# Performance work log

Hardware: AMD Instinct MI355X
Metric: run time of the kernel (lower is better)

The kernel has to match this reference:

```python
import jax, jax.numpy as jnp
import numpy as np

B, L, IN_DIMS = 256, 512, 64
UNITS, OUT_STEPS, OUT_DIMS = 256, 64, 32
KSIZE = 5


def setup_inputs() -> dict:
    key = jax.random.key(0)
    ks = jax.random.split(key, 14)
    s = lambda k, shp: jax.random.normal(k, shp, dtype=jnp.float32) * 0.05
    return {
        "inputs": jax.random.normal(ks[0], (B, L, IN_DIMS), dtype=jnp.float32),
        "conv_k": s(ks[1], (KSIZE, IN_DIMS, UNITS)),   # WIO layout
        "conv_b": s(ks[2], (UNITS,)),
        "enc_W": s(ks[3], (UNITS, 4 * UNITS)),          # kernel (input after CNN has UNITS channels)
        "enc_U": s(ks[4], (UNITS, 4 * UNITS)),          # recurrent kernel
        "enc_b": s(ks[5], (4 * UNITS,)),
        "cell_W": s(ks[6], (UNITS, 4 * UNITS)),
        "cell_U": s(ks[7], (UNITS, 4 * UNITS)),
        "cell_b": s(ks[8], (4 * UNITS,)),
        "fore_W": s(ks[9], (UNITS, OUT_DIMS)),
        "fore_b": s(ks[10], (OUT_DIMS,)),
        "back_W": s(ks[11], (UNITS, IN_DIMS)),
        "back_b": s(ks[12], (IN_DIMS,)),
    }


def _lstm_step(W, U, b, h, c, x_t):
    # Keras gate order: i, f, g(candidate), o
    z = x_t @ W + h @ U + b
    i, f, g, o = jnp.split(z, 4, axis=-1)
    c_new = jax.nn.sigmoid(f) * c + jax.nn.sigmoid(i) * jnp.tanh(g)
    h_new = jax.nn.sigmoid(o) * jnp.tanh(c_new)
    return h_new, c_new


def _forward(inputs, conv_k, conv_b, enc_W, enc_U, enc_b,
             cell_W, cell_U, cell_b, fore_W, fore_b, back_W, back_b):
    # Conv1D 'same', relu
    x = jax.lax.conv_general_dilated(
        inputs, conv_k, window_strides=(1,), padding="SAME",
        dimension_numbers=("NWC", "WIO", "NWC"))
    x = jax.nn.relu(x + conv_b)

    # Encoder LSTM (dropout inactive at inference)
    h0 = jnp.zeros((x.shape[0], UNITS), x.dtype)
    c0 = jnp.zeros((x.shape[0], UNITS), x.dtype)

    def enc_step(carry, x_t):
        h, c = carry
        h, c = _lstm_step(enc_W, enc_U, enc_b, h, c, x_t)
        return (h, c), h
    (h_T, c_T), seq = jax.lax.scan(enc_step, (h0, c0), jnp.swapaxes(x, 0, 1))
    backcast_seq = jnp.swapaxes(seq, 0, 1)  # [B, L, UNITS]

    def dec_step(carry, _):
        h, c = carry
        h, c = _lstm_step(cell_W, cell_U, cell_b, h, c, h)
        return (h, c), h
    _, outs = jax.lax.scan(dec_step, (h_T, c_T), None, length=OUT_STEPS)
    forecast_seq = jnp.swapaxes(outs, 0, 1)  # [B, OUT_STEPS, UNITS]

    forecast = forecast_seq @ fore_W + fore_b   # [B, OUT_STEPS, OUT_DIMS]
    backcast = backcast_seq @ back_W + back_b   # [B, L, IN_DIMS]
    return forecast, backcast


def reference(inputs, conv_k, conv_b, enc_W, enc_U, enc_b,
              cell_W, cell_U, cell_b, fore_W, fore_b, back_W, back_b):
    return _forward(inputs, conv_k, conv_b, enc_W, enc_U, enc_b,
                    cell_W, cell_U, cell_b, fore_W, fore_b, back_W, back_b)
```

## Files before the change

### kernel.cpp

```cpp
#include <hip/hip_runtime.h>
#include <stdint.h>

typedef unsigned short u16;
typedef __attribute__((ext_vector_type(8))) short bf16x8;
typedef __attribute__((ext_vector_type(4))) float fx4;
typedef __attribute__((ext_vector_type(2))) unsigned int u32x2;

#define MFMA16(a, b, c) __builtin_amdgcn_mfma_f32_16x16x32_bf16((a), (b), (c), 0, 0, 0)

#define OFF_X      0u
#define OFF_H      67108864u
#define RING_OFF   134348800u
#define OFF_ENCWT  142737408u
#define OFF_ENCUT  143261696u
#define OFF_CELLT  143785984u
#define OFF_CONVKT 144310272u
#define OFF_BWT    144474112u
#define OFF_FWT    144506880u
#define OFF_BAR    144523264u

#define POLL_BUDGET (1 << 25)

__device__ __forceinline__ u16 f2bf(float f) {
    uint32_t u = __builtin_bit_cast(uint32_t, f);
    u += 0x7FFFu + ((u >> 16) & 1u);
    return (u16)(u >> 16);
}
__device__ __forceinline__ float sigm(float x) { return 1.0f / (1.0f + __expf(-x)); }
__device__ __forceinline__ float tanh_f(float x) { return 1.0f - 2.0f / (__expf(2.0f * x) + 1.0f); }
__device__ __forceinline__ void vmcnt0() { asm volatile("s_waitcnt vmcnt(0)" ::: "memory"); }

__global__ void zero_kernel(unsigned char* ws) {
    int i = blockIdx.x * blockDim.x + threadIdx.x;
    uint32_t* h0 = (uint32_t*)(ws + OFF_H);
    for (int k = i; k < 32768; k += 16384) h0[k] = 0u;
    if (i < 256) ((uint32_t*)(ws + OFF_BAR))[i] = 0u;
}

__global__ void prep_kernel(const float* enc_W, const float* enc_U, const float* cell_W,
                            const float* cell_U, const float* conv_k, const float* back_W,
                            const float* fore_W, unsigned char* ws) {
    u16* encWt = (u16*)(ws + OFF_ENCWT);
    u16* encUt = (u16*)(ws + OFF_ENCUT);
    u16* cellT = (u16*)(ws + OFF_CELLT);
    u16* convKt = (u16*)(ws + OFF_CONVKT);
    u16* bwt = (u16*)(ws + OFF_BWT);
    u16* fwt = (u16*)(ws + OFF_FWT);
    int idx = blockIdx.x * blockDim.x + threadIdx.x;
    int stride = gridDim.x * blockDim.x;
    for (int i = idx; i < 262144; i += stride) {
        int n = i >> 8, k = i & 255;
        encWt[i] = f2bf(enc_W[k * 1024 + n]);
        encUt[i] = f2bf(enc_U[k * 1024 + n]);
        cellT[i] = f2bf(cell_W[k * 1024 + n] + cell_U[k * 1024 + n]);
    }
    for (int i = idx; i < 81920; i += stride) {
        int u = i / 320, rem = i - u * 320;
        convKt[i] = f2bf(conv_k[rem * 256 + u]);
    }
    for (int i = idx; i < 16384; i += stride) {
        int n = i >> 8, k = i & 255;
        bwt[i] = f2bf(back_W[k * 64 + n]);
    }
    for (int i = idx; i < 8192; i += stride) {
        int n = i >> 8, k = i & 255;
        fwt[i] = f2bf(fore_W[k * 32 + n]);
    }
}

__global__ __launch_bounds__(256) void conv_kernel(const float* __restrict__ in,
                                                   const float* __restrict__ conv_b,
                                                   unsigned char* ws) {
    const u16* kt = (const u16*)(ws + OFF_CONVKT);
    u16* xout = (u16*)(ws + OFF_X);
    int w = threadIdx.x >> 6, lane = threadIdx.x & 63;
    int m = lane & 15, q = lane >> 4;
    int mt = blockIdx.x * 4 + w;
    int r0 = mt * 16;
    int b = r0 >> 9;
    int l0 = r0 & 511;

    fx4 acc[16];
#pragma unroll
    for (int nt = 0; nt < 16; ++nt) acc[nt] = (fx4){0.f, 0.f, 0.f, 0.f};

#pragma unroll
    for (int s = 0; s < 10; ++s) {
        int k0 = s * 32 + q * 8;
        int kk = k0 >> 6, c = k0 & 63;
        int l2 = l0 + m + kk - 2;
        bf16x8 af = {0, 0, 0, 0, 0, 0, 0, 0};
        if (l2 >= 0 && l2 < 512) {
            const float* src = in + (((b << 9) + l2) << 6) + c;
            fx4 f0 = *(const fx4*)src;
            fx4 f1 = *(const fx4*)(src + 4);
            af[0] = (short)f2bf(f0[0]); af[1] = (short)f2bf(f0[1]);
            af[2] = (short)f2bf(f0[2]); af[3] = (short)f2bf(f0[3]);
            af[4] = (short)f2bf(f1[0]); af[5] = (short)f2bf(f1[1]);
            af[6] = (short)f2bf(f1[2]); af[7] = (short)f2bf(f1[3]);
        }
#pragma unroll
        for (int nt = 0; nt < 16; ++nt) {
            bf16x8 bf = *(const bf16x8*)(kt + (nt * 16 + m) * 320 + k0);
            acc[nt] = MFMA16(af, bf, acc[nt]);
        }
    }
#pragma unroll
    for (int nt = 0; nt < 16; ++nt) {
        int u = nt * 16 + m;
        float bias = conv_b[u];
#pragma unroll
        for (int r = 0; r < 4; ++r) {
            float v = acc[nt][r] + bias;
            v = v > 0.f ? v : 0.f;
            int row = r0 + q * 4 + r;
            xout[row * 256 + u] = f2bf(v);
        }
    }
}

__global__ __launch_bounds__(256, 1) void enc_fused(const float* __restrict__ enc_b,
                                                    unsigned char* ws) {
    __shared__ u16 hbuf[1024];
    int tid = threadIdx.x;
    int w = tid >> 6, lane = tid & 63, m = lane & 15, q = lane >> 4;
    int bid = blockIdx.x;
    u16* H = (u16*)(ws + OFF_H);
    int budget = POLL_BUDGET;

    if (bid >= 64) {
        int idx = bid - 64, g = idx & 15, p = idx >> 4;
        int b0 = g * 16;
        int un0 = p * 64 + w * 16;
        const u16* encWt = (const u16*)(ws + OFF_ENCWT);
        const u16* xbf = (const u16*)(ws + OFF_X);
        float* ringg = (float*)(ws + RING_OFF + (size_t)g * 524288u);
        int* hbar = (int*)(ws + OFF_BAR + g * 64);
        int* pz = (int*)(ws + OFF_BAR + g * 64 + 32);

        bf16x8 wfr[4][8];
        float bi[4];
#pragma unroll
        for (int j = 0; j < 4; ++j) {
            int row = j * 256 + un0 + m;
            bi[j] = enc_b[row];
#pragma unroll
            for (int ks = 0; ks < 8; ++ks)
                wfr[j][ks] = *(const bf16x8*)(encWt + row * 256 + ks * 32 + q * 8);
        }
        const u16* xrow = xbf + (size_t)(b0 + m) * (512 * 256) + q * 8;
        bf16x8 xa[8];
#pragma unroll
        for (int s = 0; s < 8; ++s) xa[s] = *(const bf16x8*)(xrow + s * 32);

        for (int t = 0; t < 512; ++t) {
            fx4 a0 = (fx4){bi[0], bi[0], bi[0], bi[0]};
            fx4 a1 = (fx4){bi[1], bi[1], bi[1], bi[1]};
            fx4 a2 = (fx4){bi[2], bi[2], bi[2], bi[2]};
            fx4 a3 = (fx4){bi[3], bi[3], bi[3], bi[3]};
#pragma unroll
            for (int ks = 0; ks < 8; ++ks) {
                a0 = MFMA16(xa[ks], wfr[0][ks], a0);
                a1 = MFMA16(xa[ks], wfr[1][ks], a1);
                a2 = MFMA16(xa[ks], wfr[2][ks], a2);
                a3 = MFMA16(xa[ks], wfr[3][ks], a3);
            }
            float* zs = ringg + (t & 7) * 16384 + (un0 + m) * 16 + q * 4;
            asm volatile("global_store_dwordx4 %0, %1, off sc0 sc1" :: "v"(zs), "v"(a0) : "memory");
            asm volatile("global_store_dwordx4 %0, %1, off sc0 sc1" :: "v"(zs + 4096), "v"(a1) : "memory");
            asm volatile("global_store_dwordx4 %0, %1, off sc0 sc1" :: "v"(zs + 8192), "v"(a2) : "memory");
            asm volatile("global_store_dwordx4 %0, %1, off sc0 sc1" :: "v"(zs + 12288), "v"(a3) : "memory");
            if (t < 511) {
                const u16* xA = xrow + (size_t)(t + 1) * 256;
#pragma unroll
                for (int s = 0; s < 8; ++s) xa[s] = *(const bf16x8*)(xA + s * 32);
                if (tid == 0 && t >= 7) {
                    int tgt = 4 * (t - 6);
                    while (__hip_atomic_load(hbar, __ATOMIC_RELAXED, __HIP_MEMORY_SCOPE_AGENT) < tgt
                           && --budget > 0) {}
                }
            }
            vmcnt0();
            __syncthreads();
            if (tid == 0)
                __hip_atomic_fetch_add(pz, 1, __ATOMIC_RELAXED, __HIP_MEMORY_SCOPE_AGENT);
        }
        return;
    }

    int g = bid & 15, p = bid >> 4;
    int b0 = g * 16;
    int un0 = p * 64 + w * 16;
    const u16* encUt = (const u16*)(ws + OFF_ENCUT);
    const float* ringg = (const float*)(ws + RING_OFF + (size_t)g * 524288u);
    float* csaveg = (float*)(ws + OFF_X + (size_t)g * 4194304u);
    int* hbar = (int*)(ws + OFF_BAR + g * 64);
    int* pz = (int*)(ws + OFF_BAR + g * 64 + 32);

    bf16x8 ufrag[4][8];
#pragma unroll
    for (int gi = 0; gi < 4; ++gi) {
#pragma unroll
        for (int s = 0; s < 8; ++s)
            ufrag[gi][s] = *(const bf16x8*)(encUt + (gi * 256 + un0 + m) * 256 + s * 32 + q * 8);
    }
    float creg[4] = {0.f, 0.f, 0.f, 0.f};

    for (int t = 0; t < 512; ++t) {
        if (lane == 0) {
            int tgtz = 4 * (t + 1), tgth = 4 * t;
            while (--budget > 0) {
                int vz = __hip_atomic_load(pz, __ATOMIC_RELAXED, __HIP_MEMORY_SCOPE_AGENT);
                int vh = __hip_atomic_load(hbar, __ATOMIC_RELAXED, __HIP_MEMORY_SCOPE_AGENT);
                if (vz >= tgtz && vh >= tgth) break;
            }
        }
        asm volatile("" ::: "memory");

        const u16* hA = H + (size_t)t * 65536 + (b0 + m) * 256 + q * 8;
        bf16x8 ha[8];
#pragma unroll
        for (int s = 0; s < 8; ++s) ha[s] = *(const bf16x8*)(hA + s * 32);
        const float* zb = ringg + (t & 7) * 16384 + (un0 + m) * 16 + q * 4;
        fx4 z0, z1, z2, z3;
        asm volatile("global_load_dwordx4 %0, %1, off sc0 sc1" : "=v"(z0) : "v"(zb));
        asm volatile("global_load_dwordx4 %0, %1, off sc0 sc1" : "=v"(z1) : "v"(zb + 4096));
        asm volatile("global_load_dwordx4 %0, %1, off sc0 sc1" : "=v"(z2) : "v"(zb + 8192));
        asm volatile("global_load_dwordx4 %0, %1, off sc0 sc1" : "=v"(z3) : "v"(zb + 12288));

        fx4 acc[4];
#pragma unroll
        for (int gi = 0; gi < 4; ++gi) acc[gi] = (fx4){0.f, 0.f, 0.f, 0.f};
#pragma unroll
        for (int s = 0; s < 8; ++s) {
#pragma unroll
            for (int gi = 0; gi < 4; ++gi)
                acc[gi] = MFMA16(ha[s], ufrag[gi][s], acc[gi]);
        }
        vmcnt0();
        __builtin_amdgcn_sched_barrier(0);

        float hreg[4];
#pragma unroll
        for (int r = 0; r < 4; ++r) {
            float pi = acc[0][r] + z0[r];
            float pf = acc[1][r] + z1[r];
            float pg = acc[2][r] + z2[r];
            float po = acc[3][r] + z3[r];
            float cv = sigm(pf) * creg[r] + sigm(pi) * tanh_f(pg);
            creg[r] = cv;
            hreg[r] = sigm(po) * tanh_f(cv);
        }
#pragma unroll
        for (int r = 0; r < 4; ++r)
            hbuf[(q * 4 + r) * 64 + w * 16 + m] = f2bf(hreg[r]);
        __syncthreads();
        {
            int row = tid >> 4, c4 = (tid & 15) * 4;
            u32x2 hv = *(const u32x2*)&hbuf[row * 64 + c4];
            const u16* hw = H + (size_t)(t + 1) * 65536 + (b0 + row) * 256 + p * 64 + c4;
            asm volatile("global_store_dwordx2 %0, %1, off sc0 sc1" :: "v"(hw), "v"(hv) : "memory");
        }
        vmcnt0();
        __syncthreads();
        if (tid == 0)
            __hip_atomic_fetch_add(hbar, 1, __ATOMIC_RELAXED, __HIP_MEMORY_SCOPE_AGENT);
    }

#pragma unroll
    for (int r = 0; r < 4; ++r)
        csaveg[(q * 4 + r) * 256 + un0 + m] = creg[r];
}

__global__ __launch_bounds__(256, 1) void dec_kernel(const float* __restrict__ cell_b,
                                                     unsigned char* ws) {
    int tid = threadIdx.x;
    int w = tid >> 6, lane = tid & 63, m = lane & 15, q = lane >> 4;
    int bid = blockIdx.x;
    int g = bid & 15, p = bid >> 4;
    int b0 = g * 16;
    int un0 = p * 64 + w * 16;
    int budget = POLL_BUDGET;

    const u16* cellT = (const u16*)(ws + OFF_CELLT);
    u16* H = (u16*)(ws + OFF_H);
    const float* csaveg = (const float*)(ws + OFF_X + (size_t)g * 4194304u);
    int* bar = (int*)(ws + OFF_BAR + g * 64);

    bf16x8 wfrag[4][8];
#pragma unroll
    for (int gi = 0; gi < 4; ++gi) {
#pragma unroll
        for (int s = 0; s < 8; ++s)
            wfrag[gi][s] = *(const bf16x8*)(cellT + (gi * 256 + un0 + m) * 256 + s * 32 + q * 8);
    }
    float bi[4], creg[4];
#pragma unroll
    for (int gi = 0; gi < 4; ++gi) bi[gi] = cell_b[gi * 256 + un0 + m];
#pragma unroll
    for (int r = 0; r < 4; ++r) creg[r] = csaveg[(q * 4 + r) * 256 + un0 + m];

    for (int t = 0; t < 64; ++t) {
        if (lane == 0) {
            int tgt = 2048 + 4 * t;
            while (__hip_atomic_load(bar, __ATOMIC_RELAXED, __HIP_MEMORY_SCOPE_AGENT) < tgt
                   && --budget > 0) {}
        }
        asm volatile("" ::: "memory");

        const u16* hA = H + (size_t)(512 + t) * 65536 + (b0 + m) * 256 + q * 8;
        bf16x8 ha[8];
#pragma unroll
        for (int s = 0; s < 8; ++s) ha[s] = *(const bf16x8*)(hA + s * 32);
        fx4 acc[4];
#pragma unroll
        for (int gi = 0; gi < 4; ++gi) acc[gi] = (fx4){bi[gi], bi[gi], bi[gi], bi[gi]};
#pragma unroll
        for (int s = 0; s < 8; ++s) {
#pragma unroll
            for (int gi = 0; gi < 4; ++gi)
                acc[gi] = MFMA16(ha[s], wfrag[gi][s], acc[gi]);
        }

        const u16* hw = H + (size_t)(513 + t) * 65536 + un0 + m;
#pragma unroll
        for (int r = 0; r < 4; ++r) {
            float cv = sigm(acc[1][r]) * creg[r] + sigm(acc[0][r]) * tanh_f(acc[2][r]);
            creg[r] = cv;
            float hv = sigm(acc[3][r]) * tanh_f(cv);
            uint32_t hb = (uint32_t)f2bf(hv);
            const u16* hp = hw + (b0 + q * 4 + r) * 256;
            asm volatile("global_store_short %0, %1, off sc0 sc1" :: "v"(hp), "v"(hb) : "memory");
        }
        vmcnt0();
        __syncthreads();
        if (tid == 0)
            __hip_atomic_fetch_add(bar, 1, __ATOMIC_RELAXED, __HIP_MEMORY_SCOPE_AGENT);
    }
}

__global__ __launch_bounds__(256) void out_gemm(const u16* __restrict__ A,
                                                const u16* __restrict__ Bt,
                                                const float* __restrict__ bias,
                                                float* __restrict__ out,
                                                int ncols, int seqlen) {
    int w = threadIdx.x >> 6, lane = threadIdx.x & 63, m = lane & 15, q = lane >> 4;
    int mt = blockIdx.x * 4 + w;
    int s = mt >> 4;
    int b0 = (mt & 15) * 16;
    bf16x8 af[8];
    const u16* Arow = A + ((size_t)s * 256 + b0 + m) * 256 + q * 8;
#pragma unroll
    for (int ss = 0; ss < 8; ++ss) af[ss] = *(const bf16x8*)(Arow + ss * 32);
    int ntiles = ncols >> 4;
    for (int nt = 0; nt < ntiles; ++nt) {
        fx4 acc = (fx4){0.f, 0.f, 0.f, 0.f};
#pragma unroll
        for (int ss = 0; ss < 8; ++ss) {
            bf16x8 bf = *(const bf16x8*)(Bt + (nt * 16 + m) * 256 + ss * 32 + q * 8);
            acc = MFMA16(af[ss], bf, acc);
        }
        int col = nt * 16 + m;
        float bv = bias[col];
#pragma unroll
        for (int r = 0; r < 4; ++r) {
            int b = b0 + q * 4 + r;
            out[((size_t)b * seqlen + s) * ncols + col] = acc[r] + bv;
        }
    }
}

extern "C" void kernel_launch(void* const* d_in, const int* in_sizes, int n_in,
                              void* d_out, int out_size, void* d_ws, size_t ws_size,
                              hipStream_t stream) {
    const float* inputs = (const float*)d_in[0];
    const float* conv_k = (const float*)d_in[1];
    const float* conv_b = (const float*)d_in[2];
    const float* enc_W  = (const float*)d_in[3];
    const float* enc_U  = (const float*)d_in[4];
    const float* enc_b  = (const float*)d_in[5];
    const float* cell_W = (const float*)d_in[6];
    const float* cell_U = (const float*)d_in[7];
    const float* cell_b = (const float*)d_in[8];
    const float* fore_W = (const float*)d_in[9];
    const float* fore_b = (const float*)d_in[10];
    const float* back_W = (const float*)d_in[11];
    const float* back_b = (const float*)d_in[12];
    unsigned char* ws = (unsigned char*)d_ws;
    float* out = (float*)d_out;

    zero_kernel<<<64, 256, 0, stream>>>(ws);
    prep_kernel<<<1024, 256, 0, stream>>>(enc_W, enc_U, cell_W, cell_U, conv_k, back_W, fore_W, ws);
    conv_kernel<<<2048, 256, 0, stream>>>(inputs, conv_b, ws);
    enc_fused<<<128, 256, 0, stream>>>(enc_b, ws);
    dec_kernel<<<64, 256, 0, stream>>>(cell_b, ws);

    const u16* H = (const u16*)(ws + OFF_H);
    out_gemm<<<2048, 256, 0, stream>>>(H + (size_t)1 * 65536, (const u16*)(ws + OFF_BWT),
                                       back_b, out + 524288, 64, 512);
    out_gemm<<<256, 256, 0, stream>>>(H + (size_t)513 * 65536, (const u16*)(ws + OFF_FWT),
                                      fore_b, out, 32, 64);
}
```

Before: 2.335 ms.

## Replace hidden-state barrier with tagged per-element h exchange in encoder

The recurrent encoder blocks stop waiting on a per-group hbar counter before reading h. Instead, each h value is published as a 32-bit word carrying a timestep tag in a double-buffered exchange area, and readers spin until every tag they need matches the current step. This removes the store-drain and barrier round trip on the critical path. The z ring depth is also cut from 8 to 4 slots, so the producer blocks run in tighter lockstep. In exchange it doubles h traffic, adds repeated polling reloads, and depends on relaxed ordering of plain stores for correctness.

```diff
diff --git a/kernel.cpp b/kernel.cpp
--- a/kernel.cpp
+++ b/kernel.cpp
@@ -5,12 +5,14 @@
 typedef __attribute__((ext_vector_type(8))) short bf16x8;
 typedef __attribute__((ext_vector_type(4))) float fx4;
 typedef __attribute__((ext_vector_type(2))) unsigned int u32x2;
+typedef __attribute__((ext_vector_type(4))) unsigned int u32x4;
 
 #define MFMA16(a, b, c) __builtin_amdgcn_mfma_f32_16x16x32_bf16((a), (b), (c), 0, 0, 0)
 
 #define OFF_X      0u
 #define OFF_H      67108864u
 #define RING_OFF   134348800u
+#define OFF_TEX    138543104u
 #define OFF_ENCWT  142737408u
 #define OFF_ENCUT  143261696u
 #define OFF_CELLT  143785984u
@@ -34,6 +36,11 @@
     int i = blockIdx.x * blockDim.x + threadIdx.x;
     uint32_t* h0 = (uint32_t*)(ws + OFF_H);
     for (int k = i; k < 32768; k += 16384) h0[k] = 0u;
+    uint32_t* tex = (uint32_t*)(ws + OFF_TEX);
+    for (int k = i; k < 65536; k += 16384) {
+        tex[k] = 0x00010000u;
+        tex[65536 + k] = 0u;
+    }
     if (i < 256) ((uint32_t*)(ws + OFF_BAR))[i] = 0u;
 }
 
@@ -122,6 +129,7 @@
 __global__ __launch_bounds__(256, 1) void enc_fused(const float* __restrict__ enc_b,
                                                     unsigned char* ws) {
     __shared__ u16 hbuf[1024];
+    __shared__ uint32_t hbufd[1024];
     int tid = threadIdx.x;
     int w = tid >> 6, lane = tid & 63, m = lane & 15, q = lane >> 4;
     int bid = blockIdx.x;
@@ -134,7 +142,7 @@
         int un0 = p * 64 + w * 16;
         const u16* encWt = (const u16*)(ws + OFF_ENCWT);
         const u16* xbf = (const u16*)(ws + OFF_X);
-        float* ringg = (float*)(ws + RING_OFF + (size_t)g * 524288u);
+        float* ringg = (float*)(ws + RING_OFF + (size_t)g * 262144u);
         int* hbar = (int*)(ws + OFF_BAR + g * 64);
         int* pz = (int*)(ws + OFF_BAR + g * 64 + 32);
 
@@ -165,7 +173,7 @@
                 a2 = MFMA16(xa[ks], wfr[2][ks], a2);
                 a3 = MFMA16(xa[ks], wfr[3][ks], a3);
             }
-            float* zs = ringg + (t & 7) * 16384 + (un0 + m) * 16 + q * 4;
+            float* zs = ringg + (t & 3) * 16384 + (un0 + m) * 16 + q * 4;
             asm volatile("global_store_dwordx4 %0, %1, off sc0 sc1" :: "v"(zs), "v"(a0) : "memory");
             asm volatile("global_store_dwordx4 %0, %1, off sc0 sc1" :: "v"(zs + 4096), "v"(a1) : "memory");
             asm volatile("global_store_dwordx4 %0, %1, off sc0 sc1" :: "v"(zs + 8192), "v"(a2) : "memory");
@@ -174,8 +182,8 @@
                 const u16* xA = xrow + (size_t)(t + 1) * 256;
 #pragma unroll
                 for (int s = 0; s < 8; ++s) xa[s] = *(const bf16x8*)(xA + s * 32);
-                if (tid == 0 && t >= 7) {
-                    int tgt = 4 * (t - 6);
+                if (tid == 0 && t >= 3) {
+                    int tgt = 4 * (t - 2);
                     while (__hip_atomic_load(hbar, __ATOMIC_RELAXED, __HIP_MEMORY_SCOPE_AGENT) < tgt
                            && --budget > 0) {}
                 }
@@ -192,7 +200,7 @@
     int b0 = g * 16;
     int un0 = p * 64 + w * 16;
     const u16* encUt = (const u16*)(ws + OFF_ENCUT);
-    const float* ringg = (const float*)(ws + RING_OFF + (size_t)g * 524288u);
+    const float* ringg = (const float*)(ws + RING_OFF + (size_t)g * 262144u);
     float* csaveg = (float*)(ws + OFF_X + (size_t)g * 4194304u);
     int* hbar = (int*)(ws + OFF_BAR + g * 64);
     int* pz = (int*)(ws + OFF_BAR + g * 64 + 32);
@@ -205,29 +213,61 @@
             ufrag[gi][s] = *(const bf16x8*)(encUt + (gi * 256 + un0 + m) * 256 + s * 32 + q * 8);
     }
     float creg[4] = {0.f, 0.f, 0.f, 0.f};
+    int zk = 0;
 
     for (int t = 0; t < 512; ++t) {
-        if (lane == 0) {
-            int tgtz = 4 * (t + 1), tgth = 4 * t;
+        if (lane == 0 && zk <= t) {
             while (--budget > 0) {
-                int vz = __hip_atomic_load(pz, __ATOMIC_RELAXED, __HIP_MEMORY_SCOPE_AGENT);
-                int vh = __hip_atomic_load(hbar, __ATOMIC_RELAXED, __HIP_MEMORY_SCOPE_AGENT);
-                if (vz >= tgtz && vh >= tgth) break;
+                int v = __hip_atomic_load(pz, __ATOMIC_RELAXED, __HIP_MEMORY_SCOPE_AGENT);
+                if (v >= 4 * (t + 1)) { zk = v >> 2; break; }
             }
         }
         asm volatile("" ::: "memory");
 
-        const u16* hA = H + (size_t)t * 65536 + (b0 + m) * 256 + q * 8;
-        bf16x8 ha[8];
-#pragma unroll
-        for (int s = 0; s < 8; ++s) ha[s] = *(const bf16x8*)(hA + s * 32);
-        const float* zb = ringg + (t & 7) * 16384 + (un0 + m) * 16 + q * 4;
+        const float* zb = ringg + (t & 3) * 16384 + (un0 + m) * 16 + q * 4;
         fx4 z0, z1, z2, z3;
         asm volatile("global_load_dwordx4 %0, %1, off sc0 sc1" : "=v"(z0) : "v"(zb));
         asm volatile("global_load_dwordx4 %0, %1, off sc0 sc1" : "=v"(z1) : "v"(zb + 4096));
         asm volatile("global_load_dwordx4 %0, %1, off sc0 sc1" : "=v"(z2) : "v"(zb + 8192));
         asm volatile("global_load_dwordx4 %0, %1, off sc0 sc1" : "=v"(z3) : "v"(zb + 12288));
 
+        const uint32_t* texr = (const uint32_t*)(ws + OFF_TEX + (uint32_t)(t & 1) * 262144u
+                                                 + (uint32_t)g * 16384u) + m * 256 + q * 8;
+        uint32_t expect = (uint32_t)(t + 1);
+        u32x4 ld0[8], ld1[8];
+        for (;;) {
+#pragma unroll
+            for (int s = 0; s < 8; ++s) {
+                asm volatile("global_load_dwordx4 %0, %1, off sc0 sc1"
+                             : "=v"(ld0[s]) : "v"(texr + s * 32));
+                asm volatile("global_load_dwordx4 %0, %1, off sc0 sc1"
+                             : "=v"(ld1[s]) : "v"(texr + s * 32 + 4));
+            }
+            vmcnt0();
+            int fresh = 1;
+#pragma unroll
+            for (int s = 0; s < 8; ++s) {
+                fresh &= (ld0[s][0] >> 16) == expect; fresh &= (ld0[s][1] >> 16) == expect;
+                fresh &= (ld0[s][2] >> 16) == expect; fresh &= (ld0[s][3] >> 16) == expect;
+                fresh &= (ld1[s][0] >> 16) == expect; fresh &= (ld1[s][1] >> 16) == expect;
+                fresh &= (ld1[s][2] >> 16) == expect; fresh &= (ld1[s][3] >> 16) == expect;
+            }
+            if (__all(fresh)) break;
+            if (--budget < 0) break;
+        }
+        asm volatile("" ::: "memory");
+
+        bf16x8 ha[8];
+#pragma unroll
+        for (int s = 0; s < 8; ++s) {
+            u32x4 pk;
+            pk[0] = (ld0[s][0] & 0xFFFFu) | (ld0[s][1] << 16);
+            pk[1] = (ld0[s][2] & 0xFFFFu) | (ld0[s][3] << 16);
+            pk[2] = (ld1[s][0] & 0xFFFFu) | (ld1[s][1] << 16);
+            pk[3] = (ld1[s][2] & 0xFFFFu) | (ld1[s][3] << 16);
+            ha[s] = __builtin_bit_cast(bf16x8, pk);
+        }
+
         fx4 acc[4];
 #pragma unroll
         for (int gi = 0; gi < 4; ++gi) acc[gi] = (fx4){0.f, 0.f, 0.f, 0.f};
@@ -237,8 +277,6 @@
             for (int gi = 0; gi < 4; ++gi)
                 acc[gi] = MFMA16(ha[s], ufrag[gi][s], acc[gi]);
         }
-        vmcnt0();
-        __builtin_amdgcn_sched_barrier(0);
 
         float hreg[4];
 #pragma unroll
@@ -251,18 +289,27 @@
             creg[r] = cv;
             hreg[r] = sigm(po) * tanh_f(cv);
         }
-#pragma unroll
-        for (int r = 0; r < 4; ++r)
-            hbuf[(q * 4 + r) * 64 + w * 16 + m] = f2bf(hreg[r]);
+        __syncthreads();
+        uint32_t tagw = (uint32_t)(t + 2) << 16;
+#pragma unroll
+        for (int r = 0; r < 4; ++r) {
+            int ul = w * 16 + m;
+            u16 hb = f2bf(hreg[r]);
+            hbuf[(q * 4 + r) * 64 + ul] = hb;
+            hbufd[(q * 4 + r) * 64 + ul] = tagw | (uint32_t)hb;
+        }
         __syncthreads();
         {
             int row = tid >> 4, c4 = (tid & 15) * 4;
             u32x2 hv = *(const u32x2*)&hbuf[row * 64 + c4];
             const u16* hw = H + (size_t)(t + 1) * 65536 + (b0 + row) * 256 + p * 64 + c4;
             asm volatile("global_store_dwordx2 %0, %1, off sc0 sc1" :: "v"(hw), "v"(hv) : "memory");
-        }
-        vmcnt0();
-        __syncthreads();
+            u32x4 tv = *(const u32x4*)&hbufd[row * 64 + c4];
+            uint32_t* texw = (uint32_t*)(ws + OFF_TEX + (uint32_t)((t + 1) & 1) * 262144u
+                                         + (uint32_t)g * 16384u) + row * 256 + p * 64 + c4;
+            asm volatile("global_store_dwordx4 %0, %1, off sc0 sc1" :: "v"(texw), "v"(tv) : "memory");
+        }
+        if (t == 511) vmcnt0();
         if (tid == 0)
             __hip_atomic_fetch_add(hbar, 1, __ATOMIC_RELAXED, __HIP_MEMORY_SCOPE_AGENT);
     }
```

Measured after the change: 3.585 ms. 53.5% more time.

## Replace atomic counter barrier with per-producer flag slots polled by vector load

Applied to the files above, without the earlier changes.

Swaps the shared atomic fetch-add counter used for the h-step barrier between recurrent blocks for per-block flag words in an 8-slot ring. Each producer stores its step number with a plain store, and consumers poll all four flags with one dwordx4 load. The z-ring wait in the recurrent blocks now caches the observed producer count, so it skips re-polling until that count falls behind. This targets atomic RMW contention and latency on the serial critical path. It reuses the conv-kernel weight region for the flags, which adds an extra zeroing launch and relies on that region being dead by then.

```diff
diff --git a/kernel.cpp b/kernel.cpp
--- a/kernel.cpp
+++ b/kernel.cpp
@@ -5,6 +5,7 @@
 typedef __attribute__((ext_vector_type(8))) short bf16x8;
 typedef __attribute__((ext_vector_type(4))) float fx4;
 typedef __attribute__((ext_vector_type(2))) unsigned int u32x2;
+typedef __attribute__((ext_vector_type(4))) unsigned int u32x4;
 
 #define MFMA16(a, b, c) __builtin_amdgcn_mfma_f32_16x16x32_bf16((a), (b), (c), 0, 0, 0)
 
@@ -18,6 +19,7 @@
 #define OFF_BWT    144474112u
 #define OFF_FWT    144506880u
 #define OFF_BAR    144523264u
+#define OFF_FLG2   (OFF_CONVKT)
 
 #define POLL_BUDGET (1 << 25)
 
@@ -29,12 +31,28 @@
 __device__ __forceinline__ float sigm(float x) { return 1.0f / (1.0f + __expf(-x)); }
 __device__ __forceinline__ float tanh_f(float x) { return 1.0f - 2.0f / (__expf(2.0f * x) + 1.0f); }
 __device__ __forceinline__ void vmcnt0() { asm volatile("s_waitcnt vmcnt(0)" ::: "memory"); }
+
+__device__ __forceinline__ u32x4 ld_flags4(const void* p) {
+    u32x4 v;
+    asm volatile("global_load_dwordx4 %0, %1, off sc0 sc1\ns_waitcnt vmcnt(0)"
+                 : "=v"(v) : "v"(p) : "memory");
+    return v;
+}
+__device__ __forceinline__ void st_flag(void* p, uint32_t v) {
+    asm volatile("global_store_dword %0, %1, off sc0 sc1" :: "v"(p), "v"(v) : "memory");
+}
 
 __global__ void zero_kernel(unsigned char* ws) {
     int i = blockIdx.x * blockDim.x + threadIdx.x;
     uint32_t* h0 = (uint32_t*)(ws + OFF_H);
     for (int k = i; k < 32768; k += 16384) h0[k] = 0u;
     if (i < 256) ((uint32_t*)(ws + OFF_BAR))[i] = 0u;
+}
+
+__global__ void zero2_kernel(unsigned char* ws) {
+    uint32_t* p = (uint32_t*)(ws + OFF_FLG2);
+    int i = threadIdx.x;
+    for (int k = i; k < 512; k += 256) p[k] = 0u;
 }
 
 __global__ void prep_kernel(const float* enc_W, const float* enc_U, const float* cell_W,
@@ -135,7 +153,6 @@
         const u16* encWt = (const u16*)(ws + OFF_ENCWT);
         const u16* xbf = (const u16*)(ws + OFF_X);
         float* ringg = (float*)(ws + RING_OFF + (size_t)g * 524288u);
-        int* hbar = (int*)(ws + OFF_BAR + g * 64);
         int* pz = (int*)(ws + OFF_BAR + g * 64 + 32);
 
         bf16x8 wfr[4][8];
@@ -175,9 +192,15 @@
 #pragma unroll
                 for (int s = 0; s < 8; ++s) xa[s] = *(const bf16x8*)(xA + s * 32);
                 if (tid == 0 && t >= 7) {
-                    int tgt = 4 * (t - 6);
-                    while (__hip_atomic_load(hbar, __ATOMIC_RELAXED, __HIP_MEMORY_SCOPE_AGENT) < tgt
-                           && --budget > 0) {}
+                    int need = t - 6;
+                    const void* fl = ws + OFF_FLG2 + (uint32_t)g * 128u
+                                     + (uint32_t)(need & 7) * 16u;
+                    for (;;) {
+                        u32x4 f = ld_flags4(fl);
+                        if ((int)f[0] >= need && (int)f[1] >= need &&
+                            (int)f[2] >= need && (int)f[3] >= need) break;
+                        if (--budget < 0) break;
+                    }
                 }
             }
             vmcnt0();
@@ -194,7 +217,6 @@
     const u16* encUt = (const u16*)(ws + OFF_ENCUT);
     const float* ringg = (const float*)(ws + RING_OFF + (size_t)g * 524288u);
     float* csaveg = (float*)(ws + OFF_X + (size_t)g * 4194304u);
-    int* hbar = (int*)(ws + OFF_BAR + g * 64);
     int* pz = (int*)(ws + OFF_BAR + g * 64 + 32);
 
     bf16x8 ufrag[4][8];
@@ -205,14 +227,22 @@
             ufrag[gi][s] = *(const bf16x8*)(encUt + (gi * 256 + un0 + m) * 256 + s * 32 + q * 8);
     }
     float creg[4] = {0.f, 0.f, 0.f, 0.f};
+    int zk = 0;
 
     for (int t = 0; t < 512; ++t) {
-        if (lane == 0) {
-            int tgtz = 4 * (t + 1), tgth = 4 * t;
+        if (lane == 0 && zk <= t) {
             while (--budget > 0) {
-                int vz = __hip_atomic_load(pz, __ATOMIC_RELAXED, __HIP_MEMORY_SCOPE_AGENT);
-                int vh = __hip_atomic_load(hbar, __ATOMIC_RELAXED, __HIP_MEMORY_SCOPE_AGENT);
-                if (vz >= tgtz && vh >= tgth) break;
+                int v = __hip_atomic_load(pz, __ATOMIC_RELAXED, __HIP_MEMORY_SCOPE_AGENT);
+                if (v >= 4 * (t + 1)) { zk = v >> 2; break; }
+            }
+        }
+        if (t > 0 && lane == 0) {
+            const void* fl = ws + OFF_FLG2 + (uint32_t)g * 128u + (uint32_t)(t & 7) * 16u;
+            for (;;) {
+                u32x4 f = ld_flags4(fl);
+                if ((int)f[0] >= t && (int)f[1] >= t &&
+                    (int)f[2] >= t && (int)f[3] >= t) break;
+                if (--budget < 0) break;
             }
         }
         asm volatile("" ::: "memory");
@@ -263,8 +293,11 @@
         }
         vmcnt0();
         __syncthreads();
-        if (tid == 0)
-            __hip_atomic_fetch_add(hbar, 1, __ATOMIC_RELAXED, __HIP_MEMORY_SCOPE_AGENT);
+        if (tid == 0) {
+            void* myf = ws + OFF_FLG2 + (uint32_t)g * 128u
+                        + (uint32_t)((t + 1) & 7) * 16u + (uint32_t)p * 4u;
+            st_flag(myf, (uint32_t)(t + 1));
+        }
     }
 
 #pragma unroll
@@ -285,7 +318,6 @@
     const u16* cellT = (const u16*)(ws + OFF_CELLT);
     u16* H = (u16*)(ws + OFF_H);
     const float* csaveg = (const float*)(ws + OFF_X + (size_t)g * 4194304u);
-    int* bar = (int*)(ws + OFF_BAR + g * 64);
 
     bf16x8 wfrag[4][8];
 #pragma unroll
@@ -301,14 +333,19 @@
     for (int r = 0; r < 4; ++r) creg[r] = csaveg[(q * 4 + r) * 256 + un0 + m];
 
     for (int t = 0; t < 64; ++t) {
-        if (lane == 0) {
-            int tgt = 2048 + 4 * t;
-            while (__hip_atomic_load(bar, __ATOMIC_RELAXED, __HIP_MEMORY_SCOPE_AGENT) < tgt
-                   && --budget > 0) {}
+        int T = 512 + t;
+        if (t > 0 && lane == 0) {
+            const void* fl = ws + OFF_FLG2 + (uint32_t)g * 128u + (uint32_t)(T & 7) * 16u;
+            for (;;) {
+                u32x4 f = ld_flags4(fl);
+                if ((int)f[0] >= T && (int)f[1] >= T &&
+                    (int)f[2] >= T && (int)f[3] >= T) break;
+                if (--budget < 0) break;
+            }
         }
         asm volatile("" ::: "memory");
 
-        const u16* hA = H + (size_t)(512 + t) * 65536 + (b0 + m) * 256 + q * 8;
+        const u16* hA = H + (size_t)T * 65536 + (b0 + m) * 256 + q * 8;
         bf16x8 ha[8];
 #pragma unroll
         for (int s = 0; s < 8; ++s) ha[s] = *(const bf16x8*)(hA + s * 32);
@@ -322,7 +359,7 @@
                 acc[gi] = MFMA16(ha[s], wfrag[gi][s], acc[gi]);
         }
 
-        const u16* hw = H + (size_t)(513 + t) * 65536 + un0 + m;
+        const u16* hw = H + (size_t)(T + 1) * 65536 + un0 + m;
 #pragma unroll
         for (int r = 0; r < 4; ++r) {
             float cv = sigm(acc[1][r]) * creg[r] + sigm(acc[0][r]) * tanh_f(acc[2][r]);
@@ -334,8 +371,11 @@
         }
         vmcnt0();
         __syncthreads();
-        if (tid == 0)
-            __hip_atomic_fetch_add(bar, 1, __ATOMIC_RELAXED, __HIP_MEMORY_SCOPE_AGENT);
+        if (tid == 0) {
+            void* myf = ws + OFF_FLG2 + (uint32_t)g * 128u
+                        + (uint32_t)((T + 1) & 7) * 16u + (uint32_t)p * 4u;
+            st_flag(myf, (uint32_t)(T + 1));
+        }
     }
 }
 
@@ -392,6 +432,7 @@
     zero_kernel<<<64, 256, 0, stream>>>(ws);
     prep_kernel<<<1024, 256, 0, stream>>>(enc_W, enc_U, cell_W, cell_U, conv_k, back_W, fore_W, ws);
     conv_kernel<<<2048, 256, 0, stream>>>(inputs, conv_b, ws);
+    zero2_kernel<<<1, 256, 0, stream>>>(ws);
     enc_fused<<<128, 256, 0, stream>>>(enc_b, ws);
     dec_kernel<<<64, 256, 0, stream>>>(cell_b, ws);
 
```

Measured after the change: 2.323 ms. Within noise of the previous version (-0.5%).
